# Kernel optimization log

Hardware: AMD Instinct MI355X
Metric: run time of the kernel (lower is better)

The kernel has to match this reference:

```python
import jax, jax.numpy as jnp
import numpy as np

B, C, H, W = 8, 64, 128, 128
K = 3            # deformable kernel size
DIL = 1          # dilation == padding for the deformable conv
OFF_K = 2 * (DIL + 1) + 1   # = 5, offset-conv kernel
OFF_PAD = DIL + 1            # = 2, same-padding for offset conv
KK = K * K


def setup_inputs() -> dict:
    key = jax.random.key(0)
    k1, k2, k3, k4 = jax.random.split(key, 4)
    x = jax.random.normal(k1, (B, C, H, W), dtype=jnp.float32)
    weights = jax.random.normal(k2, (C, C, K, K), dtype=jnp.float32) * 0.05
    offset_w = jax.random.normal(k3, (2 * KK, C, OFF_K, OFF_K), dtype=jnp.float32) * 0.02
    offset_b = jax.random.normal(k4, (2 * KK,), dtype=jnp.float32) * 0.01
    return {"x": x, "weights": weights, "offset_w": offset_w, "offset_b": offset_b}


def _deform_conv2d(x, weights, off):
    # x: [B,C,H,W]; weights: [O,C,K,K]; off: [B,2*KK,H,W] (dy,dx interleaved per tap)
    b, c, h, w = x.shape
    o = weights.shape[0]
    off = off.reshape(b, KK, 2, h, w)
    dy = off[:, :, 0]            # [B,KK,H,W]
    dx = off[:, :, 1]
    ti = jnp.arange(KK) // K     # kernel row per tap
    tj = jnp.arange(KK) % K      # kernel col per tap
    ygrid = jnp.arange(h, dtype=jnp.float32)
    xgrid = jnp.arange(w, dtype=jnp.float32)
    # sample position: out_pos - pad + tap*dilation + offset
    base_y = (ti * DIL - DIL).astype(jnp.float32)  # pad = DIL
    base_x = (tj * DIL - DIL).astype(jnp.float32)
    py = ygrid[None, None, :, None] + base_y[None, :, None, None] + dy  # [B,KK,H,W]
    px = xgrid[None, None, None, :] + base_x[None, :, None, None] + dx

    def sample_one(img, py_b, px_b):
        # img: [C,H,W]; py_b/px_b: [KK,H,W] -> [C,KK,H,W]
        y0 = jnp.floor(py_b)
        x0 = jnp.floor(px_b)
        fy = py_b - y0
        fx = px_b - x0
        y0i = y0.astype(jnp.int32)
        x0i = x0.astype(jnp.int32)

        def corner(yi, xi, wgt):
            valid = (yi >= 0) & (yi < h) & (xi >= 0) & (xi < w)
            v = img[:, jnp.clip(yi, 0, h - 1), jnp.clip(xi, 0, w - 1)]  # [C,KK,H,W]
            return v * (wgt * valid)[None]

        return (corner(y0i, x0i, (1 - fy) * (1 - fx))
                + corner(y0i, x0i + 1, (1 - fy) * fx)
                + corner(y0i + 1, x0i, fy * (1 - fx))
                + corner(y0i + 1, x0i + 1, fy * fx))

    sampled = jax.vmap(sample_one)(x, py, px)            # [B,C,KK,H,W]
    return jnp.einsum('bctyx,oct->boyx', sampled, weights.reshape(o, c, KK))


def reference(x, weights, offset_w, offset_b):
    # offset conv (same padding) + Hardtanh clamp to [-1,1]
    off = jax.lax.conv_general_dilated(
        x, offset_w, window_strides=(1, 1),
        padding=[(OFF_PAD, OFF_PAD), (OFF_PAD, OFF_PAD)],
        dimension_numbers=('NCHW', 'OIHW', 'NCHW'))
    off = off + offset_b[None, :, None, None]
    off = jnp.clip(off, -1.0, 1.0)
    return _deform_conv2d(x, weights, off)
```

## Files before the change

kernel.cpp:

```cpp
#include <hip/hip_runtime.h>

#define BB  8
#define CC  64
#define HH  128
#define WW  128
#define OCC 18
#define XP  133
#define SP  72
#define XTP 68

typedef __attribute__((ext_vector_type(8)))  short bf16x8;
typedef __attribute__((ext_vector_type(16))) float f32x16;

static __device__ __forceinline__ ushort f2bf(float f) {
    union { float f; unsigned u; } v; v.f = f;
    unsigned r = (v.u + 0x7FFFu + ((v.u >> 16) & 1u)) >> 16;
    return (ushort)r;
}
static __device__ __forceinline__ float bfu(unsigned u) {
    union { unsigned u; float f; } v; v.u = u; return v.f;
}

__global__ __launch_bounds__(256) void prep_kernel(
    const float* __restrict__ x, const float* __restrict__ w,
    const float* __restrict__ ow, ushort* __restrict__ XT,
    ushort* __restrict__ WAf, ushort* __restrict__ WDf)
{
    __shared__ ushort T[64 * XTP];
    const int tid = threadIdx.x;
    const int phys = blockIdx.x;

    if (phys >= 2 * BB * HH) {
        int id = phys - 2 * BB * HH;
        if (id < 200) {
            int idx = id * 256 + tid;
            int j  = idx & 7;
            int l  = (idx >> 3) & 63;
            int cs = (idx >> 9) & 3;
            int t  = idx >> 11;
            int oc = l & 31;
            int c  = cs * 16 + (l >> 5) * 8 + j;
            float v = (oc < OCC) ? ow[((size_t)(oc * CC + c)) * 25 + t] : 0.f;
            WAf[idx] = f2bf(v);
        } else {
            int idx = (id - 200) * 256 + tid;
            int j  = idx & 7;
            int l  = (idx >> 3) & 63;
            int cs = (idx >> 9) & 3;
            int mt = (idx >> 11) & 1;
            int t  = idx >> 12;
            int o  = mt * 32 + (l & 31);
            int c  = cs * 16 + (l >> 5) * 8 + j;
            WDf[idx] = f2bf(w[((size_t)(o * CC + c)) * 9 + t]);
        }
        return;
    }

    const int b    = phys & 7;
    const int idx  = phys >> 3;
    const int half = idx & 1;
    const int y    = idx >> 1;

    {
        int j = idx * 256 + tid;
        if (j < 5 * XP * 8) {
            int r   = j / (XP * 8);
            int off = j % (XP * 8);
            int yp  = (r < 2) ? r : (128 + r);
            ((uint4*)(XT + ((size_t)b * XP + yp) * XP * 64))[off] = make_uint4(0, 0, 0, 0);
        }
    }

    const int p   = tid & 63;
    const int ch4 = tid >> 6;
    const float* xb = x + (size_t)b * CC * HH * WW + (size_t)y * WW + half * 64;
#pragma unroll
    for (int i = 0; i < 16; i++) {
        int c = i * 4 + ch4;
        T[p * XTP + c] = f2bf(xb[(size_t)c * HH * WW + p]);
    }
    __syncthreads();

    ushort* orow = XT + (((size_t)b * XP + (y + 2)) * XP) * 64;

    if (half == 0) {
        if (tid < 16) {
            int col = tid >> 3;
            ((uint4*)(orow + (size_t)col * 64))[tid & 7] = make_uint4(0, 0, 0, 0);
        }
    } else {
        if (tid < 24) {
            int col = 130 + (tid >> 3);
            ((uint4*)(orow + (size_t)col * 64))[tid & 7] = make_uint4(0, 0, 0, 0);
        }
    }

#pragma unroll
    for (int g = 0; g < 2; g++) {
        int i2 = g * 256 + tid;
        int pl = i2 >> 3;
        int part = i2 & 7;
        uint2 lo = *(const uint2*)&T[pl * XTP + part * 8];
        uint2 hi = *(const uint2*)&T[pl * XTP + part * 8 + 4];
        uint4 wv; wv.x = lo.x; wv.y = lo.y; wv.z = hi.x; wv.w = hi.y;
        ((uint4*)(orow + ((size_t)(half * 64 + pl + 2)) * 64))[part] = wv;
    }
}

__global__ __launch_bounds__(256, 6) void fused_kernel(
    const ushort* __restrict__ XT, const ushort* __restrict__ WAf,
    const ushort* __restrict__ WDf, const float* __restrict__ ob,
    float* __restrict__ out)
{
    __shared__ __align__(16) char smem[68 * SP * 2];
    __shared__ float off_lds[OCC * 64];

    const int tid   = threadIdx.x;
    const int lane  = tid & 63;
    const int n     = lane & 31;
    const int h     = lane >> 5;
    const int w     = tid >> 6;
    const int ptile = w & 1;
    const int tset  = w >> 1;

    const int b    = blockIdx.x & 7;
    const int idx  = blockIdx.x >> 3;
    const int half = idx & 1;
    const int y    = idx >> 1;

    {
        ushort* XROW = (ushort*)smem;
        float*  red  = (float*)smem;
        f32x16 acc = {};
        const ushort* src0 = XT + (((size_t)b * XP + y) * XP + half * 64) * 64;

        for (int ky = 0; ky < 5; ky++) {
            if (ky) __syncthreads();
            const ushort* src = src0 + (size_t)ky * XP * 64;
            for (int i = tid; i < 68 * 8; i += 256) {
                int pl = i >> 3, ch = (i & 7) * 8;
                *(uint4*)&XROW[pl * SP + ch] = *(const uint4*)(src + (size_t)pl * 64 + ch);
            }
            __syncthreads();

#pragma unroll
            for (int kx = 0; kx < 5; kx++) {
                const int t = ky * 5 + kx;
                const ushort* bbase = &XROW[(ptile * 32 + n + kx) * SP + h * 8];
#pragma unroll
                for (int c2 = 0; c2 < 2; c2++) {
                    const int cs = tset * 2 + c2;
                    bf16x8 af = *(const bf16x8*)(WAf + (((size_t)t * 4 + cs) * 64 + lane) * 8);
                    bf16x8 bf = *(const bf16x8*)(bbase + cs * 16);
                    acc = __builtin_amdgcn_mfma_f32_32x32x16_bf16(af, bf, acc, 0, 0, 0);
                }
            }
        }
        __syncthreads();
        if (tset == 1) {
#pragma unroll
            for (int r = 0; r < 16; r++)
                red[ptile * 1024 + r * 64 + lane] = acc[r];
        }
        __syncthreads();
        if (tset == 0) {
#pragma unroll
            for (int r = 0; r < 16; r++) {
                int oc = (r & 3) + 8 * (r >> 2) + 4 * h;
                if (oc < OCC) {
                    float v = acc[r] + red[ptile * 1024 + r * 64 + lane] + ob[oc];
                    v = fminf(fmaxf(v, -1.f), 1.f);
                    off_lds[oc * 64 + ptile * 32 + n] = v;
                }
            }
        }
        __syncthreads();
    }

    ushort* S = (ushort*)smem;
    const int p   = tid >> 2;
    const int cs4 = (tid & 3) * 16;

    const int m0 = ptile * 32;
    const int n0 = tset * 32;

    f32x16 acc = {};
    const ushort* xtb = XT + (size_t)b * XP * XP * 64;

    for (int t = 0; t < 9; t++) {
        float dy = off_lds[(2 * t) * 64 + p];
        float dx = off_lds[(2 * t + 1) * 64 + p];
        float py = (float)(y + t / 3 - 1) + dy;
        float px = (float)(half * 64 + p + t % 3 - 1) + dx;
        float y0f = floorf(py), x0f = floorf(px);
        float fy = py - y0f, fx = px - x0f;
        int iy = (int)y0f + 2, ix = (int)x0f + 2;
        float w00 = (1.f - fy) * (1.f - fx), w01 = (1.f - fy) * fx;
        float w10 = fy * (1.f - fx),         w11 = fy * fx;

        const ushort* c00 = xtb + ((size_t)iy * XP + ix) * 64 + cs4;
        const ushort* c10 = c00 + XP * 64;

        uint4 q[8];
        q[0] = *(const uint4*)(c00);      q[1] = *(const uint4*)(c00 + 8);
        q[2] = *(const uint4*)(c00 + 64); q[3] = *(const uint4*)(c00 + 72);
        q[4] = *(const uint4*)(c10);      q[5] = *(const uint4*)(c10 + 8);
        q[6] = *(const uint4*)(c10 + 64); q[7] = *(const uint4*)(c10 + 72);

        __syncthreads();

#pragma unroll
        for (int m = 0; m < 2; m++) {
            unsigned o4[4];
#pragma unroll
            for (int j = 0; j < 4; j++) {
                unsigned u00 = ((const unsigned*)&q[m])[j];
                unsigned u01 = ((const unsigned*)&q[2 + m])[j];
                unsigned u10 = ((const unsigned*)&q[4 + m])[j];
                unsigned u11 = ((const unsigned*)&q[6 + m])[j];
                float lo = w00 * bfu(u00 << 16) + w01 * bfu(u01 << 16)
                         + w10 * bfu(u10 << 16) + w11 * bfu(u11 << 16);
                float hi = w00 * bfu(u00 & 0xffff0000u) + w01 * bfu(u01 & 0xffff0000u)
                         + w10 * bfu(u10 & 0xffff0000u) + w11 * bfu(u11 & 0xffff0000u);
                o4[j] = (unsigned)f2bf(lo) | ((unsigned)f2bf(hi) << 16);
            }
            *(uint4*)&S[p * SP + cs4 + m * 8] = *(uint4*)o4;
        }
        __syncthreads();

        const ushort* bp = &S[(n0 + n) * SP + h * 8];
#pragma unroll
        for (int cs = 0; cs < 4; cs++) {
            bf16x8 af = *(const bf16x8*)(WDf + ((((size_t)t * 2 + ptile) * 4 + cs) * 64 + lane) * 8);
            bf16x8 bf = *(const bf16x8*)(bp + cs * 16);
            acc = __builtin_amdgcn_mfma_f32_32x32x16_bf16(af, bf, acc, 0, 0, 0);
        }
    }

#pragma unroll
    for (int r = 0; r < 16; r++) {
        int o = m0 + (r & 3) + 8 * (r >> 2) + 4 * h;
        out[((size_t)(b * CC + o) * HH + y) * WW + half * 64 + n0 + n] = acc[r];
    }
}

extern "C" void kernel_launch(void* const* d_in, const int* in_sizes, int n_in,
                              void* d_out, int out_size, void* d_ws, size_t ws_size,
                              hipStream_t stream)
{
    const float* x  = (const float*)d_in[0];
    const float* w  = (const float*)d_in[1];
    const float* ow = (const float*)d_in[2];
    const float* ob = (const float*)d_in[3];
    float* out = (float*)d_out;

    ushort* XT  = (ushort*)d_ws;
    ushort* WAf = (ushort*)((char*)d_ws + 18113536);
    ushort* WDf = (ushort*)((char*)d_ws + 18215936);

    prep_kernel<<<2 * BB * HH + 344, 256, 0, stream>>>(x, w, ow, XT, WAf, WDf);
    fused_kernel<<<2 * BB * HH, 256, 0, stream>>>(XT, WAf, WDf, ob, out);
}
```

Baseline: 146.7 us.

## Apply bilinear weights after MFMA per corner instead of interpolating before GEMM

The deformable stage no longer builds a bilinear-interpolated bf16 tile in LDS. Each wave feeds the four raw corner pixels from the transposed input straight into MFMAs and scales each corner's partial product by its bilinear weight in registers. This drops the LDS staging, the per-tap block barriers and the interpolation ALU work, at the cost of four times more MFMA work and more scattered global loads. The block now covers a full 128-pixel row with each wave owning 32 pixels for all 64 output channels, which also removes the cross-wave reduction in the offset conv. Occupancy drops because launch bounds go to 2 and register pressure rises with two accumulators.

```diff
diff --git a/kernel.cpp b/kernel.cpp
--- a/kernel.cpp
+++ b/kernel.cpp
@@ -16,9 +16,6 @@
     union { float f; unsigned u; } v; v.f = f;
     unsigned r = (v.u + 0x7FFFu + ((v.u >> 16) & 1u)) >> 16;
     return (ushort)r;
-}
-static __device__ __forceinline__ float bfu(unsigned u) {
-    union { unsigned u; float f; } v; v.u = u; return v.f;
 }
 
 __global__ __launch_bounds__(256) void prep_kernel(
@@ -107,37 +104,56 @@
     }
 }
 
-__global__ __launch_bounds__(256, 6) void fused_kernel(
+static __device__ __forceinline__ void corner_mma(
+    const ushort* cp, float wgt, const bf16x8* a0, const bf16x8* a1,
+    const f32x16& kZero, f32x16& acc0, f32x16& acc1)
+{
+    bf16x8 b0 = *(const bf16x8*)(cp);
+    bf16x8 b1 = *(const bf16x8*)(cp + 16);
+    bf16x8 b2 = *(const bf16x8*)(cp + 32);
+    bf16x8 b3 = *(const bf16x8*)(cp + 48);
+    f32x16 p0 = __builtin_amdgcn_mfma_f32_32x32x16_bf16(a0[0], b0, kZero, 0, 0, 0);
+    f32x16 p1 = __builtin_amdgcn_mfma_f32_32x32x16_bf16(a1[0], b0, kZero, 0, 0, 0);
+    p0 = __builtin_amdgcn_mfma_f32_32x32x16_bf16(a0[1], b1, p0, 0, 0, 0);
+    p1 = __builtin_amdgcn_mfma_f32_32x32x16_bf16(a1[1], b1, p1, 0, 0, 0);
+    p0 = __builtin_amdgcn_mfma_f32_32x32x16_bf16(a0[2], b2, p0, 0, 0, 0);
+    p1 = __builtin_amdgcn_mfma_f32_32x32x16_bf16(a1[2], b2, p1, 0, 0, 0);
+    p0 = __builtin_amdgcn_mfma_f32_32x32x16_bf16(a0[3], b3, p0, 0, 0, 0);
+    p1 = __builtin_amdgcn_mfma_f32_32x32x16_bf16(a1[3], b3, p1, 0, 0, 0);
+#pragma unroll
+    for (int r = 0; r < 16; r++) {
+        acc0[r] += wgt * p0[r];
+        acc1[r] += wgt * p1[r];
+    }
+}
+
+__global__ __launch_bounds__(256, 2) void fused_kernel(
     const ushort* __restrict__ XT, const ushort* __restrict__ WAf,
     const ushort* __restrict__ WDf, const float* __restrict__ ob,
     float* __restrict__ out)
 {
-    __shared__ __align__(16) char smem[68 * SP * 2];
-    __shared__ float off_lds[OCC * 64];
-
-    const int tid   = threadIdx.x;
-    const int lane  = tid & 63;
-    const int n     = lane & 31;
-    const int h     = lane >> 5;
-    const int w     = tid >> 6;
-    const int ptile = w & 1;
-    const int tset  = w >> 1;
-
-    const int b    = blockIdx.x & 7;
-    const int idx  = blockIdx.x >> 3;
-    const int half = idx & 1;
-    const int y    = idx >> 1;
+    __shared__ __align__(16) ushort XROW[132 * SP];
+    __shared__ float off_lds[OCC * 128];
+
+    const int tid  = threadIdx.x;
+    const int lane = tid & 63;
+    const int n    = lane & 31;
+    const int h    = lane >> 5;
+    const int wv   = tid >> 6;
+    const int n0   = wv * 32;
+    const int px   = n0 + n;
+
+    const int b = blockIdx.x & 7;
+    const int y = blockIdx.x >> 3;
 
     {
-        ushort* XROW = (ushort*)smem;
-        float*  red  = (float*)smem;
         f32x16 acc = {};
-        const ushort* src0 = XT + (((size_t)b * XP + y) * XP + half * 64) * 64;
+        const ushort* src0 = XT + (((size_t)b * XP + y) * XP) * 64;
 
         for (int ky = 0; ky < 5; ky++) {
             if (ky) __syncthreads();
             const ushort* src = src0 + (size_t)ky * XP * 64;
-            for (int i = tid; i < 68 * 8; i += 256) {
+            for (int i = tid; i < 132 * 8; i += 256) {
                 int pl = i >> 3, ch = (i & 7) * 8;
                 *(uint4*)&XROW[pl * SP + ch] = *(const uint4*)(src + (size_t)pl * 64 + ch);
             }
@@ -146,101 +162,63 @@
 #pragma unroll
             for (int kx = 0; kx < 5; kx++) {
                 const int t = ky * 5 + kx;
-                const ushort* bbase = &XROW[(ptile * 32 + n + kx) * SP + h * 8];
-#pragma unroll
-                for (int c2 = 0; c2 < 2; c2++) {
-                    const int cs = tset * 2 + c2;
+                const ushort* bbase = &XROW[(px + kx) * SP + h * 8];
+#pragma unroll
+                for (int cs = 0; cs < 4; cs++) {
                     bf16x8 af = *(const bf16x8*)(WAf + (((size_t)t * 4 + cs) * 64 + lane) * 8);
                     bf16x8 bf = *(const bf16x8*)(bbase + cs * 16);
                     acc = __builtin_amdgcn_mfma_f32_32x32x16_bf16(af, bf, acc, 0, 0, 0);
                 }
             }
         }
-        __syncthreads();
-        if (tset == 1) {
-#pragma unroll
-            for (int r = 0; r < 16; r++)
-                red[ptile * 1024 + r * 64 + lane] = acc[r];
-        }
-        __syncthreads();
-        if (tset == 0) {
-#pragma unroll
-            for (int r = 0; r < 16; r++) {
-                int oc = (r & 3) + 8 * (r >> 2) + 4 * h;
-                if (oc < OCC) {
-                    float v = acc[r] + red[ptile * 1024 + r * 64 + lane] + ob[oc];
-                    v = fminf(fmaxf(v, -1.f), 1.f);
-                    off_lds[oc * 64 + ptile * 32 + n] = v;
-                }
+
+#pragma unroll
+        for (int r = 0; r < 16; r++) {
+            int oc = (r & 3) + 8 * (r >> 2) + 4 * h;
+            if (oc < OCC) {
+                float v = acc[r] + ob[oc];
+                off_lds[oc * 128 + px] = fminf(fmaxf(v, -1.f), 1.f);
             }
         }
-        __syncthreads();
-    }
-
-    ushort* S = (ushort*)smem;
-    const int p   = tid >> 2;
-    const int cs4 = (tid & 3) * 16;
-
-    const int m0 = ptile * 32;
-    const int n0 = tset * 32;
-
-    f32x16 acc = {};
+    }
+
+    f32x16 acc0 = {}, acc1 = {};
+    f32x16 kZero = {};
     const ushort* xtb = XT + (size_t)b * XP * XP * 64;
 
     for (int t = 0; t < 9; t++) {
-        float dy = off_lds[(2 * t) * 64 + p];
-        float dx = off_lds[(2 * t + 1) * 64 + p];
-        float py = (float)(y + t / 3 - 1) + dy;
-        float px = (float)(half * 64 + p + t % 3 - 1) + dx;
-        float y0f = floorf(py), x0f = floorf(px);
-        float fy = py - y0f, fx = px - x0f;
+        float dy = off_lds[(2 * t) * 128 + px];
+        float dx = off_lds[(2 * t + 1) * 128 + px];
+        float py  = (float)(y + t / 3 - 1) + dy;
+        float pxf = (float)(px + t % 3 - 1) + dx;
+        float y0f = floorf(py), x0f = floorf(pxf);
+        float fy = py - y0f, fx = pxf - x0f;
         int iy = (int)y0f + 2, ix = (int)x0f + 2;
         float w00 = (1.f - fy) * (1.f - fx), w01 = (1.f - fy) * fx;
         float w10 = fy * (1.f - fx),         w11 = fy * fx;
 
-        const ushort* c00 = xtb + ((size_t)iy * XP + ix) * 64 + cs4;
-        const ushort* c10 = c00 + XP * 64;
-
-        uint4 q[8];
-        q[0] = *(const uint4*)(c00);      q[1] = *(const uint4*)(c00 + 8);
-        q[2] = *(const uint4*)(c00 + 64); q[3] = *(const uint4*)(c00 + 72);
-        q[4] = *(const uint4*)(c10);      q[5] = *(const uint4*)(c10 + 8);
-        q[6] = *(const uint4*)(c10 + 64); q[7] = *(const uint4*)(c10 + 72);
-
-        __syncthreads();
-
-#pragma unroll
-        for (int m = 0; m < 2; m++) {
-            unsigned o4[4];
-#pragma unroll
-            for (int j = 0; j < 4; j++) {
-                unsigned u00 = ((const unsigned*)&q[m])[j];
-                unsigned u01 = ((const unsigned*)&q[2 + m])[j];
-                unsigned u10 = ((const unsigned*)&q[4 + m])[j];
-                unsigned u11 = ((const unsigned*)&q[6 + m])[j];
-                float lo = w00 * bfu(u00 << 16) + w01 * bfu(u01 << 16)
-                         + w10 * bfu(u10 << 16) + w11 * bfu(u11 << 16);
-                float hi = w00 * bfu(u00 & 0xffff0000u) + w01 * bfu(u01 & 0xffff0000u)
-                         + w10 * bfu(u10 & 0xffff0000u) + w11 * bfu(u11 & 0xffff0000u);
-                o4[j] = (unsigned)f2bf(lo) | ((unsigned)f2bf(hi) << 16);
-            }
-            *(uint4*)&S[p * SP + cs4 + m * 8] = *(uint4*)o4;
-        }
-        __syncthreads();
-
-        const ushort* bp = &S[(n0 + n) * SP + h * 8];
+        bf16x8 a0[4], a1[4];
 #pragma unroll
         for (int cs = 0; cs < 4; cs++) {
-            bf16x8 af = *(const bf16x8*)(WDf + ((((size_t)t * 2 + ptile) * 4 + cs) * 64 + lane) * 8);
-            bf16x8 bf = *(const bf16x8*)(bp + cs * 16);
-            acc = __builtin_amdgcn_mfma_f32_32x32x16_bf16(af, bf, acc, 0, 0, 0);
-        }
+            a0[cs] = *(const bf16x8*)(WDf + (((size_t)(t * 2 + 0) * 4 + cs) * 64 + lane) * 8);
+            a1[cs] = *(const bf16x8*)(WDf + (((size_t)(t * 2 + 1) * 4 + cs) * 64 + lane) * 8);
+        }
+
+        const ushort* c00 = xtb + ((size_t)iy * XP + ix) * 64 + h * 8;
+        const ushort* c10 = c00 + (size_t)XP * 64;
+
+        corner_mma(c00,      w00, a0, a1, kZero, acc0, acc1);
+        corner_mma(c00 + 64, w01, a0, a1, kZero, acc0, acc1);
+        corner_mma(c10,      w10, a0, a1, kZero, acc0, acc1);
+        corner_mma(c10 + 64, w11, a0, a1, kZero, acc0, acc1);
     }
 
 #pragma unroll
     for (int r = 0; r < 16; r++) {
-        int o = m0 + (r & 3) + 8 * (r >> 2) + 4 * h;
-        out[((size_t)(b * CC + o) * HH + y) * WW + half * 64 + n0 + n] = acc[r];
+        int o = (r & 3) + 8 * (r >> 2) + 4 * h;
+        float* orow = out + ((size_t)(b * CC + o) * HH + y) * WW + px;
+        orow[0] = acc0[r];
+        orow[(size_t)32 * HH * WW] = acc1[r];
     }
 }
 
@@ -259,5 +237,5 @@
     ushort* WDf = (ushort*)((char*)d_ws + 18215936);
 
     prep_kernel<<<2 * BB * HH + 344, 256, 0, stream>>>(x, w, ow, XT, WAf, WDf);
-    fused_kernel<<<2 * BB * HH, 256, 0, stream>>>(XT, WAf, WDf, ob, out);
-}
+    fused_kernel<<<BB * HH, 256, 0, stream>>>(XT, WAf, WDf, ob, out);
+}
```

Result: slower. 192.8 us (+31.4%).
